# Kernel optimization log

Measured on AMD Instinct MI355X. Metric: run time of the kernel, lower is better.

## Reference

```python
import jax, jax.numpy as jnp
import numpy as np

D_K = 8192   # sequence length (module calls it d_k)
D_MODEL = 128

def setup_inputs() -> dict:
    key = jax.random.key(0)
    k1, k2, k3 = jax.random.split(key, 3)
    Q = jax.random.normal(k1, (D_K, D_MODEL), dtype=jnp.float32)
    K = jax.random.normal(k2, (D_K, D_MODEL), dtype=jnp.float32)
    V = jax.random.normal(k3, (D_K, D_MODEL), dtype=jnp.float32)
    return {"Q": Q, "K": K, "V": V}

def reference(Q, K, V):
    # scores: [d_k, d_k] -- full attention matrix, scaled by 1/sqrt(d_k)
    # (faithful to the source: scale uses d_k, the sequence dim)
    inv_scale = 1.0 / jnp.sqrt(jnp.asarray(D_K, dtype=Q.dtype))
    scores = jnp.einsum('qd,kd->qk', Q, K) * inv_scale
    attn = jax.nn.softmax(scores, axis=-1)
    return jnp.einsum('qk,kd->qd', attn, V)
```

## Files before the change

kernel.cpp:

```cpp
#include <hip/hip_runtime.h>

#define SEQ 8192
#define DM  128
#define KS  8

typedef __attribute__((ext_vector_type(8)))  short bf16x8;
typedef __attribute__((ext_vector_type(16))) float f32x16;
typedef __attribute__((ext_vector_type(2)))  unsigned int uintx2;

static __device__ __forceinline__ unsigned short f2bf(float f) {
    unsigned int u = __builtin_bit_cast(unsigned int, f);
    u += 0x7FFFu + ((u >> 16) & 1u);
    return (unsigned short)(u >> 16);
}
static __device__ __forceinline__ unsigned int pack2bf(float a, float b) {
    return ((unsigned int)f2bf(b) << 16) | (unsigned int)f2bf(a);
}
static __device__ __forceinline__ float bflo(unsigned int u) {
    return __builtin_bit_cast(float, u << 16);
}
static __device__ __forceinline__ float bfhi(unsigned int u) {
    return __builtin_bit_cast(float, u & 0xFFFF0000u);
}
static __device__ __forceinline__ bf16x8 as_frag(uint4 v) {
    return __builtin_bit_cast(bf16x8, v);
}
static __device__ __forceinline__ unsigned int pack2bf_trunc(float a, float b) {
    return __builtin_amdgcn_perm(__builtin_bit_cast(unsigned int, b),
                                 __builtin_bit_cast(unsigned int, a), 0x07060302u);
}
static __device__ __forceinline__ void gl_lds16(const void* g, void* l) {
    __builtin_amdgcn_global_load_lds(
        (const __attribute__((address_space(1))) void*)(unsigned long long)g,
        (__attribute__((address_space(3))) void*)(unsigned int)(unsigned long long)l,
        16, 0, 0);
}
#define CL2 (1.4426950408889634f / 90.50966799187809f)

__global__ __launch_bounds__(512) void prep_kernel(
        const float* __restrict__ Q, const float* __restrict__ K,
        const float* __restrict__ V,
        uint2* __restrict__ Qb2, uint4* __restrict__ Kt, uint4* __restrict__ Vt) {
    __shared__ float VL[32 * 132 + 4];
    const int b = blockIdx.x, tid = threadIdx.x;
    const float4* Q4 = (const float4*)Q;
    const float4* K4 = (const float4*)K;
    const float4* V4 = (const float4*)V;

    #pragma unroll
    for (int u = 0; u < 2; ++u) {
        int f4 = u * 512 + tid;
        int k = f4 >> 5, c4 = f4 & 31;
        float4 v = V4[(size_t)b * 1024 + f4];
        *(float4*)(VL + k * 132 + c4 * 4) = v;
    }
    #pragma unroll
    for (int u = 0; u < 2; ++u) {
        int f4 = u * 512 + tid;
        float4 v = Q4[(size_t)b * 1024 + f4];
        Qb2[(size_t)b * 1024 + f4] = make_uint2(pack2bf(v.x * CL2, v.y * CL2),
                                                pack2bf(v.z * CL2, v.w * CL2));
    }
    {
        int p = tid;
        int q = p & 31, h = (p >> 5) & 1, s = p >> 6;
        int fi = (b * 32 + q) * 32 + s * 4 + h * 2;
        float4 a = K4[fi], c = K4[fi + 1];
        Kt[(size_t)b * 512 + p] = make_uint4(pack2bf(a.x, a.y), pack2bf(a.z, a.w),
                                             pack2bf(c.x, c.y), pack2bf(c.z, c.w));
    }
    __syncthreads();
    {
        int p = tid;
        int q = p & 31, h = (p >> 5) & 1, w = p >> 6;
        int d = (w >> 1) * 32 + q;
        int k0 = (w & 1) * 16 + h * 8;
        unsigned int r[4];
        #pragma unroll
        for (int jj = 0; jj < 4; ++jj) {
            float e0 = VL[(k0 + 2 * jj) * 132 + d];
            float e1 = VL[(k0 + 2 * jj + 1) * 132 + d];
            r[jj] = pack2bf(e0, e1);
        }
        Vt[(size_t)b * 512 + p] = make_uint4(r[0], r[1], r[2], r[3]);
    }
}

__global__ __launch_bounds__(512, 2) void attn_kernel(
        const unsigned short* __restrict__ Qb,
        const uint4* __restrict__ Kt,
        const uint4* __restrict__ Vt,
        uint2* __restrict__ Opart, float* __restrict__ Lpart) {
    __shared__ __align__(16) char smem[65536];
    __shared__ float Lx[128];
    const int tid = threadIdx.x;
    const int wid = tid >> 6, lane = tid & 63;
    const int i = wid & 3, j = wid >> 2;
    const int q = lane & 31, h = lane >> 5;
    const int qt = blockIdx.x & 63, ks = blockIdx.x >> 6;
    const int qbase = qt * 128 + i * 32;
    const int tile0 = ks * 32 + j * 16;

    uint4 qf[8];
    {
        const unsigned short* qrow = Qb + (qbase + q) * DM + 8 * h;
        #pragma unroll
        for (int s = 0; s < 8; ++s) qf[s] = *(const uint4*)(qrow + 16 * s);
    }

    f32x16 oacc[4];
    #pragma unroll
    for (int mb = 0; mb < 4; ++mb)
        #pragma unroll
        for (int r = 0; r < 16; ++r) oacc[mb][r] = 0.f;
    float ls0 = 0.f, ls1 = 0.f, ls2 = 0.f, ls3 = 0.f;

    char* const mybuf = smem + j * 32768;
    auto stage = [&](int buf, int tile) {
        char* base = mybuf + buf * 16384;
        const uint4* kt = Kt + (size_t)tile * 512;
        const uint4* vt = Vt + (size_t)tile * 512;
        #pragma unroll
        for (int u = 0; u < 2; ++u) {
            int ki = i * 2 + u;
            gl_lds16(kt + ki * 64 + lane, base + ki * 1024);
            gl_lds16(vt + ki * 64 + lane, base + 8192 + ki * 1024);
        }
    };

    stage(0, tile0);
    #pragma unroll 1
    for (int t = 0; t < 16; ++t) {
        __syncthreads();
        if (t < 15) stage((t + 1) & 1, tile0 + t + 1);
        const char* kl = mybuf + (t & 1) * 16384 + lane * 16;

        uint4 kf[8];
        #pragma unroll
        for (int s = 0; s < 8; ++s) kf[s] = *(const uint4*)(kl + s * 1024);

        f32x16 sa, sb;
        #pragma unroll
        for (int r = 0; r < 16; ++r) { sa[r] = 0.f; sb[r] = 0.f; }
        __builtin_amdgcn_s_setprio(1);
        #pragma unroll
        for (int s = 0; s < 4; ++s) {
            sa = __builtin_amdgcn_mfma_f32_32x32x16_bf16(
                     as_frag(kf[s]), as_frag(qf[s]), sa, 0, 0, 0);
            sb = __builtin_amdgcn_mfma_f32_32x32x16_bf16(
                     as_frag(kf[s + 4]), as_frag(qf[s + 4]), sb, 0, 0, 0);
        }
        __builtin_amdgcn_s_setprio(0);

        uint4 vf[8];
        #pragma unroll
        for (int w = 0; w < 8; ++w) vf[w] = *(const uint4*)(kl + 8192 + w * 1024);

        float p[16];
        #pragma unroll
        for (int r = 0; r < 16; ++r) p[r] = __builtin_amdgcn_exp2f(sa[r] + sb[r]);
        #pragma unroll
        for (int r = 0; r < 4; ++r) {
            ls0 += p[4 * r + 0]; ls1 += p[4 * r + 1];
            ls2 += p[4 * r + 2]; ls3 += p[4 * r + 3];
        }
        unsigned int pk[8];
        #pragma unroll
        for (int jj = 0; jj < 8; ++jj) pk[jj] = pack2bf_trunc(p[2 * jj], p[2 * jj + 1]);
        uint4 B0, B1;
        {
            uintx2 r0 = __builtin_amdgcn_permlane32_swap(pk[0], pk[2], false, false);
            uintx2 r1 = __builtin_amdgcn_permlane32_swap(pk[1], pk[3], false, false);
            uintx2 r4 = __builtin_amdgcn_permlane32_swap(pk[4], pk[6], false, false);
            uintx2 r5 = __builtin_amdgcn_permlane32_swap(pk[5], pk[7], false, false);
            B0.x = r0[0];  B0.z = r0[1];
            B0.y = r1[0];  B0.w = r1[1];
            B1.x = r4[0];  B1.z = r4[1];
            B1.y = r5[0];  B1.w = r5[1];
        }

        __builtin_amdgcn_s_setprio(1);
        #pragma unroll
        for (int mb = 0; mb < 4; ++mb) {
            oacc[mb] = __builtin_amdgcn_mfma_f32_32x32x16_bf16(
                           as_frag(vf[mb * 2 + 0]), as_frag(B0), oacc[mb], 0, 0, 0);
            oacc[mb] = __builtin_amdgcn_mfma_f32_32x32x16_bf16(
                           as_frag(vf[mb * 2 + 1]), as_frag(B1), oacc[mb], 0, 0, 0);
        }
        __builtin_amdgcn_s_setprio(0);
    }
    float lsum = (ls0 + ls1) + (ls2 + ls3);

    float l2 = lsum + __shfl_xor(lsum, 32);
    __syncthreads();
    float* Lg = (float*)(smem + i * 16384);
    if (j == 0) {
        #pragma unroll
        for (int mb = 0; mb < 4; ++mb)
            #pragma unroll
            for (int r = 0; r < 16; ++r) {
                int dl = 32 * mb + (r & 3) + 8 * (r >> 2) + 4 * h;
                Lg[dl * 32 + q] = oacc[mb][r];
            }
        if (h == 0) Lx[i * 32 + q] = l2;
    }
    __syncthreads();
    if (j == 1) {
        #pragma unroll
        for (int mb = 0; mb < 4; ++mb)
            #pragma unroll
            for (int r = 0; r < 16; ++r) {
                int dl = 32 * mb + (r & 3) + 8 * (r >> 2) + 4 * h;
                Lg[dl * 32 + q] += oacc[mb][r];
            }
        if (h == 0) Lpart[(size_t)ks * SEQ + qbase + q] = Lx[i * 32 + q] + l2;
    }
    __syncthreads();
    #pragma unroll
    for (int u = 0; u < 8; ++u) {
        int idx = u * 512 + tid;
        int rd = idx >> 5, c4 = idx & 31;
        int ig = c4 >> 3, q4 = c4 & 7;
        float4 v = *(const float4*)(smem + ig * 16384 + (rd * 8 + q4) * 16);
        Opart[(((size_t)(ks * 64 + qt)) * 128 + rd) * 32 + c4] =
            make_uint2(pack2bf(v.x, v.y), pack2bf(v.z, v.w));
    }
}

__global__ __launch_bounds__(512) void reduce_kernel(
        const uint2* __restrict__ Opart, const float* __restrict__ Lpart,
        float* __restrict__ Out) {
    __shared__ float T[32 * 132 + 4];
    __shared__ float Rinv[128];
    const int tid = threadIdx.x;
    const int qt = blockIdx.x & 63, dq = blockIdx.x >> 6;
    if (tid < 128) {
        float L = 0.f;
        #pragma unroll
        for (int ks = 0; ks < KS; ++ks) L += Lpart[(size_t)ks * SEQ + qt * 128 + tid];
        Rinv[tid] = 1.0f / L;
    }
    const int c = tid & 31, dsub = tid >> 5;
    float4 acc[2];
    #pragma unroll
    for (int rr = 0; rr < 2; ++rr) { acc[rr].x = acc[rr].y = acc[rr].z = acc[rr].w = 0.f; }
    #pragma unroll
    for (int ks = 0; ks < KS; ++ks) {
        #pragma unroll
        for (int rr = 0; rr < 2; ++rr) {
            int d_l = rr * 16 + dsub;
            uint2 w = Opart[(((size_t)(ks * 64 + qt)) * 128 + dq * 32 + d_l) * 32 + c];
            acc[rr].x += bflo(w.x); acc[rr].y += bfhi(w.x);
            acc[rr].z += bflo(w.y); acc[rr].w += bfhi(w.y);
        }
    }
    #pragma unroll
    for (int rr = 0; rr < 2; ++rr)
        *(float4*)(T + (rr * 16 + dsub) * 132 + c * 4) = acc[rr];
    __syncthreads();
    const int q_l = tid >> 2, part = tid & 3;
    float r = Rinv[q_l];
    #pragma unroll
    for (int g = 0; g < 2; ++g) {
        int d0 = part * 8 + g * 4;
        float4 o;
        o.x = T[(d0 + 0) * 132 + q_l] * r;
        o.y = T[(d0 + 1) * 132 + q_l] * r;
        o.z = T[(d0 + 2) * 132 + q_l] * r;
        o.w = T[(d0 + 3) * 132 + q_l] * r;
        *(float4*)(Out + ((size_t)(qt * 128 + q_l)) * DM + dq * 32 + d0) = o;
    }
}

extern "C" void kernel_launch(void* const* d_in, const int* in_sizes, int n_in,
                              void* d_out, int out_size, void* d_ws, size_t ws_size,
                              hipStream_t stream) {
    const float* Q = (const float*)d_in[0];
    const float* K = (const float*)d_in[1];
    const float* V = (const float*)d_in[2];
    char* ws = (char*)d_ws;
    uint2* Qb2  = (uint2*)ws;
    uint4* Kt   = (uint4*)(ws + 2 * 1024 * 1024);
    uint4* Vt   = (uint4*)(ws + 4 * 1024 * 1024);
    float* Lpart= (float*)(ws + 6 * 1024 * 1024);
    uint2* Opart= (uint2*)(ws + 6 * 1024 * 1024 + 262144);
    float* Out  = (float*)d_out;

    prep_kernel<<<256, 512, 0, stream>>>(Q, K, V, Qb2, Kt, Vt);
    attn_kernel<<<512, 512, 0, stream>>>((const unsigned short*)Qb2, Kt, Vt,
                                         Opart, Lpart);
    reduce_kernel<<<256, 512, 0, stream>>>(Opart, Lpart, Out);
}
```

Baseline: 112.4 us.

## Split keys across blocks instead of intra-block warp groups, doubling KS to 16

Removes the in-block split of the key range between two warp groups and gives each key split its own 256-thread block, so the grid doubles to 1024 blocks with half the shared memory each. The in-block LDS reduction of partial outputs goes away and each block writes its own partial output and row sum. The cost is twice the partial-output and row-sum traffic to global memory, plus a reduce kernel that now sums 16 partials instead of 8.

```diff
diff --git a/kernel.cpp b/kernel.cpp
--- a/kernel.cpp
+++ b/kernel.cpp
@@ -2,7 +2,7 @@
 
 #define SEQ 8192
 #define DM  128
-#define KS  8
+#define KS  16
 
 typedef __attribute__((ext_vector_type(8)))  short bf16x8;
 typedef __attribute__((ext_vector_type(16))) float f32x16;
@@ -86,20 +86,19 @@
     }
 }
 
-__global__ __launch_bounds__(512, 2) void attn_kernel(
+__global__ __launch_bounds__(256, 4) void attn_kernel(
         const unsigned short* __restrict__ Qb,
         const uint4* __restrict__ Kt,
         const uint4* __restrict__ Vt,
         uint2* __restrict__ Opart, float* __restrict__ Lpart) {
-    __shared__ __align__(16) char smem[65536];
-    __shared__ float Lx[128];
+    __shared__ __align__(16) char smem[32768];
     const int tid = threadIdx.x;
     const int wid = tid >> 6, lane = tid & 63;
-    const int i = wid & 3, j = wid >> 2;
+    const int i = wid;
     const int q = lane & 31, h = lane >> 5;
     const int qt = blockIdx.x & 63, ks = blockIdx.x >> 6;
     const int qbase = qt * 128 + i * 32;
-    const int tile0 = ks * 32 + j * 16;
+    const int tile0 = ks * 16;
 
     uint4 qf[8];
     {
@@ -115,9 +114,8 @@
         for (int r = 0; r < 16; ++r) oacc[mb][r] = 0.f;
     float ls0 = 0.f, ls1 = 0.f, ls2 = 0.f, ls3 = 0.f;
 
-    char* const mybuf = smem + j * 32768;
     auto stage = [&](int buf, int tile) {
-        char* base = mybuf + buf * 16384;
+        char* base = smem + buf * 16384;
         const uint4* kt = Kt + (size_t)tile * 512;
         const uint4* vt = Vt + (size_t)tile * 512;
         #pragma unroll
@@ -133,7 +131,7 @@
     for (int t = 0; t < 16; ++t) {
         __syncthreads();
         if (t < 15) stage((t + 1) & 1, tile0 + t + 1);
-        const char* kl = mybuf + (t & 1) * 16384 + lane * 16;
+        const char* kl = smem + (t & 1) * 16384 + lane * 16;
 
         uint4 kf[8];
         #pragma unroll
@@ -192,38 +190,31 @@
     float lsum = (ls0 + ls1) + (ls2 + ls3);
 
     float l2 = lsum + __shfl_xor(lsum, 32);
-    __syncthreads();
-    float* Lg = (float*)(smem + i * 16384);
-    if (j == 0) {
-        #pragma unroll
-        for (int mb = 0; mb < 4; ++mb)
+    if (h == 0) Lpart[(size_t)ks * SEQ + qbase + q] = l2;
+
+    #pragma unroll
+    for (int pass = 0; pass < 2; ++pass) {
+        __syncthreads();
+        if ((i >> 1) == pass) {
+            float* Lg = (float*)(smem + (i & 1) * 16384);
             #pragma unroll
-            for (int r = 0; r < 16; ++r) {
-                int dl = 32 * mb + (r & 3) + 8 * (r >> 2) + 4 * h;
-                Lg[dl * 32 + q] = oacc[mb][r];
-            }
-        if (h == 0) Lx[i * 32 + q] = l2;
-    }
-    __syncthreads();
-    if (j == 1) {
-        #pragma unroll
-        for (int mb = 0; mb < 4; ++mb)
-            #pragma unroll
-            for (int r = 0; r < 16; ++r) {
-                int dl = 32 * mb + (r & 3) + 8 * (r >> 2) + 4 * h;
-                Lg[dl * 32 + q] += oacc[mb][r];
-            }
-        if (h == 0) Lpart[(size_t)ks * SEQ + qbase + q] = Lx[i * 32 + q] + l2;
-    }
-    __syncthreads();
-    #pragma unroll
-    for (int u = 0; u < 8; ++u) {
-        int idx = u * 512 + tid;
-        int rd = idx >> 5, c4 = idx & 31;
-        int ig = c4 >> 3, q4 = c4 & 7;
-        float4 v = *(const float4*)(smem + ig * 16384 + (rd * 8 + q4) * 16);
-        Opart[(((size_t)(ks * 64 + qt)) * 128 + rd) * 32 + c4] =
-            make_uint2(pack2bf(v.x, v.y), pack2bf(v.z, v.w));
+            for (int mb = 0; mb < 4; ++mb)
+                #pragma unroll
+                for (int r = 0; r < 16; ++r) {
+                    int dl = 32 * mb + (r & 3) + 8 * (r >> 2) + 4 * h;
+                    Lg[dl * 32 + q] = oacc[mb][r];
+                }
+        }
+        __syncthreads();
+        #pragma unroll
+        for (int u = 0; u < 8; ++u) {
+            int idx = u * 256 + tid;
+            int rd = idx >> 4, c4l = idx & 15;
+            int ig = c4l >> 3, q4 = c4l & 7;
+            float4 v = *(const float4*)(smem + ig * 16384 + (rd * 8 + q4) * 16);
+            Opart[(((size_t)(ks * 64 + qt)) * 128 + rd) * 32 + pass * 16 + c4l] =
+                make_uint2(pack2bf(v.x, v.y), pack2bf(v.z, v.w));
+        }
     }
 }
 
@@ -283,11 +274,11 @@
     uint4* Kt   = (uint4*)(ws + 2 * 1024 * 1024);
     uint4* Vt   = (uint4*)(ws + 4 * 1024 * 1024);
     float* Lpart= (float*)(ws + 6 * 1024 * 1024);
-    uint2* Opart= (uint2*)(ws + 6 * 1024 * 1024 + 262144);
+    uint2* Opart= (uint2*)(ws + 6 * 1024 * 1024 + 524288);
     float* Out  = (float*)d_out;
 
     prep_kernel<<<256, 512, 0, stream>>>(Q, K, V, Qb2, Kt, Vt);
-    attn_kernel<<<512, 512, 0, stream>>>((const unsigned short*)Qb2, Kt, Vt,
-                                         Opart, Lpart);
+    attn_kernel<<<1024, 256, 0, stream>>>((const unsigned short*)Qb2, Kt, Vt,
+                                          Opart, Lpart);
     reduce_kernel<<<256, 512, 0, stream>>>(Opart, Lpart, Out);
 }
```

Result: slower. 269.3 us (+139.7%).
